# Performance work log

Hardware: AMD Instinct MI355X
Metric: run time of the kernel (lower is better)

## Reference

```python
import jax, jax.numpy as jnp
import numpy as np

B, S, H, F = 4, 2048, 1024, 4096
E, K = 8, 2


def setup_inputs() -> dict:
    key = jax.random.key(0)
    ks = jax.random.split(key, 8)
    s1 = 1.0 / np.sqrt(H)
    s2 = 1.0 / np.sqrt(F)
    return {
        "hidden_states": jax.random.normal(ks[0], (B, S, H), dtype=jnp.float32),
        "w1": jax.random.normal(ks[1], (E, H, F), dtype=jnp.float32) * s1,
        "b1": jnp.zeros((E, F), dtype=jnp.float32),
        "w2": jax.random.normal(ks[2], (E, F, H), dtype=jnp.float32) * s2,
        "b2": jnp.zeros((E, H), dtype=jnp.float32),
        "router_w": jax.random.normal(ks[3], (H, E), dtype=jnp.float32) * s1,
        "router_b": jnp.zeros((E,), dtype=jnp.float32),
    }


def reference(hidden_states, w1, b1, w2, b2, router_w, router_b):
    b, s, h = hidden_states.shape
    x = hidden_states.reshape(-1, h)              # [T, H]
    # --- router: softmax over expert logits, top-k, renormalize ---
    logits = x @ router_w + router_b              # [T, E]
    probs = jax.nn.softmax(logits, axis=-1)
    top_w, top_i = jax.lax.top_k(probs, K)        # [T, K]
    top_w = top_w / jnp.sum(top_w, axis=-1, keepdims=True)
    # --- dispatch/combine: per-expert FFN, weighted sum (same math as
    # gather/scatter loop in the torch module, expressed densely per expert) ---
    out = jnp.zeros_like(x)
    for e in range(E):
        we = jnp.sum(jnp.where(top_i == e, top_w, 0.0), axis=-1)   # [T]
        he = jax.nn.gelu(x @ w1[e] + b1[e]) @ w2[e] + b2[e]        # [T, H]
        out = out + we[:, None] * he
    return out.reshape(b, s, h)
```

## Files before the change

kernel.cpp:

```cpp
#include <hip/hip_runtime.h>
#include <cstdint>
#include <cstddef>

#define T_TOK 8192
#define HD 1024
#define FD 4096
#define NE 8
#define RCAP 17408

typedef __bf16 bf16_t;
typedef __bf16 bf16x8 __attribute__((ext_vector_type(8)));
typedef __bf16 bf16x4 __attribute__((ext_vector_type(4)));
typedef float floatx4 __attribute__((ext_vector_type(4)));

#define BM 128
#define BN 128
#define BK 64
#define LDS_STRIDE 72

__device__ __forceinline__ float gelu_tanh(float x) {
    float x3 = x * x * x;
    float t = tanhf(0.7978845608028654f * (x + 0.044715f * x3));
    return 0.5f * x * (1.0f + t);
}

__global__ __launch_bounds__(256) void transpose_conv_kernel(
    const float* __restrict__ in, bf16_t* __restrict__ out, int R, int C)
{
    __shared__ float tile[32][33];
    const int e = blockIdx.z;
    const int c0 = blockIdx.x * 32;
    const int r0 = blockIdx.y * 32;
    const float* src = in + (size_t)e * R * C;
    bf16_t* dst = out + (size_t)e * R * C;
    const int tx = threadIdx.x & 31;
    const int ty = threadIdx.x >> 5;
    #pragma unroll
    for (int i = ty; i < 32; i += 8)
        tile[i][tx] = src[(size_t)(r0 + i) * C + c0 + tx];
    __syncthreads();
    #pragma unroll
    for (int i = ty; i < 32; i += 8)
        dst[(size_t)(c0 + i) * R + r0 + tx] = (bf16_t)tile[tx][i];
}

__global__ __launch_bounds__(256) void router_kernel(
    const float* __restrict__ x, const float* __restrict__ rw,
    const float* __restrict__ rb,
    int* __restrict__ tok_e, float* __restrict__ tok_w, int* __restrict__ counts)
{
    const int t = blockIdx.x * 4 + (threadIdx.x >> 6);
    const int lane = threadIdx.x & 63;
    const float* xr = x + (size_t)t * HD;
    float acc[NE];
    #pragma unroll
    for (int e = 0; e < NE; ++e) acc[e] = 0.f;
    #pragma unroll 4
    for (int i = 0; i < HD / 64; ++i) {
        int h = lane + 64 * i;
        float xv = xr[h];
        const float4* w4 = (const float4*)(rw + (size_t)h * NE);
        float4 wa = w4[0], wb = w4[1];
        acc[0] += xv * wa.x; acc[1] += xv * wa.y;
        acc[2] += xv * wa.z; acc[3] += xv * wa.w;
        acc[4] += xv * wb.x; acc[5] += xv * wb.y;
        acc[6] += xv * wb.z; acc[7] += xv * wb.w;
    }
    #pragma unroll
    for (int s = 32; s > 0; s >>= 1)
        #pragma unroll
        for (int e = 0; e < NE; ++e)
            acc[e] += __shfl_xor(acc[e], s, 64);
    if (lane == 0) {
        float l[NE];
        #pragma unroll
        for (int e = 0; e < NE; ++e) l[e] = acc[e] + rb[e];
        int e1 = 0;
        #pragma unroll
        for (int e = 1; e < NE; ++e) if (l[e] > l[e1]) e1 = e;
        int e2 = (e1 == 0) ? 1 : 0;
        #pragma unroll
        for (int e = 0; e < NE; ++e) {
            if (e == e1 || e == e2) continue;
            if (l[e] > l[e2]) e2 = e;
        }
        float m = l[e1];
        float q1 = 1.0f;
        float q2 = expf(l[e2] - m);
        float inv = 1.0f / (q1 + q2);
        tok_e[t * 2]     = e1;
        tok_e[t * 2 + 1] = e2;
        tok_w[t * 2]     = q1 * inv;
        tok_w[t * 2 + 1] = q2 * inv;
        atomicAdd(&counts[e1], 1);
        atomicAdd(&counts[e2], 1);
    }
}

__global__ void offsets_kernel(const int* __restrict__ counts,
                               int* __restrict__ offsets, int* __restrict__ cursors)
{
    if (threadIdx.x == 0) {
        int cum = 0;
        for (int e = 0; e < NE; ++e) {
            offsets[e] = cum;
            cursors[e] = cum;
            cum += (counts[e] + BM - 1) & ~(BM - 1);
        }
    }
}

__global__ __launch_bounds__(256) void gather_kernel(
    const float* __restrict__ x, const int* __restrict__ tok_e,
    const float* __restrict__ tok_w, int* __restrict__ cursors,
    bf16_t* __restrict__ Xg, int* __restrict__ rows_token, float* __restrict__ rows_w)
{
    const int pair = blockIdx.x * 4 + (threadIdx.x >> 6);
    const int lane = threadIdx.x & 63;
    const int t = pair >> 1;
    int pos;
    if (lane == 0) {
        int e = tok_e[pair];
        pos = atomicAdd(&cursors[e], 1);
        rows_token[pos] = t;
        rows_w[pos] = tok_w[pair];
    }
    pos = __shfl(pos, 0, 64);
    const float4* src = (const float4*)(x + (size_t)t * HD);
    bf16_t* dst = Xg + (size_t)pos * HD;
    #pragma unroll
    for (int i = 0; i < HD / 256; ++i) {
        float4 v = src[lane + 64 * i];
        int base = (lane + 64 * i) * 4;
        bf16x4 o;
        o[0] = (bf16_t)v.x; o[1] = (bf16_t)v.y;
        o[2] = (bf16_t)v.z; o[3] = (bf16_t)v.w;
        *(bf16x4*)(dst + base) = o;
    }
}

template<int KDIM>
__device__ __forceinline__ void gemm_tile(
    const bf16_t* __restrict__ aG,
    const bf16_t* __restrict__ bG,
    bf16_t As[BM][LDS_STRIDE], bf16_t Bs[BN][LDS_STRIDE],
    floatx4 acc[4][4])
{
    const int tid = threadIdx.x;
    const int lane = tid & 63;
    const int wave = tid >> 6;
    const int quad = lane >> 4;
    const int l16 = lane & 15;
    const int wm = (wave & 1) * 64;
    const int wn = (wave >> 1) * 64;
    const int r0 = tid >> 3;
    const int c0 = (tid & 7) * 8;

    for (int k0 = 0; k0 < KDIM; k0 += BK) {
        #pragma unroll
        for (int p = 0; p < 4; ++p) {
            int r = p * 32 + r0;
            *(bf16x8*)(&As[r][c0]) = *(const bf16x8*)(aG + (size_t)r * KDIM + k0 + c0);
            *(bf16x8*)(&Bs[r][c0]) = *(const bf16x8*)(bG + (size_t)r * KDIM + k0 + c0);
        }
        __syncthreads();
        #pragma unroll
        for (int kk = 0; kk < BK; kk += 32) {
            bf16x8 af[4], bfr[4];
            #pragma unroll
            for (int i = 0; i < 4; ++i)
                af[i] = *(const bf16x8*)(&As[wm + i * 16 + l16][kk + quad * 8]);
            #pragma unroll
            for (int i = 0; i < 4; ++i)
                bfr[i] = *(const bf16x8*)(&Bs[wn + i * 16 + l16][kk + quad * 8]);
            #pragma unroll
            for (int i = 0; i < 4; ++i)
                #pragma unroll
                for (int j = 0; j < 4; ++j)
                    acc[i][j] = __builtin_amdgcn_mfma_f32_16x16x32_bf16(
                        af[i], bfr[j], acc[i][j], 0, 0, 0);
        }
        __syncthreads();
    }
}

__global__ __launch_bounds__(256) void ffn1_kernel(
    const bf16_t* __restrict__ Xg, const bf16_t* __restrict__ w1t,
    const float* __restrict__ b1, bf16_t* __restrict__ Hb,
    const int* __restrict__ counts, const int* __restrict__ offsets)
{
    const int e = blockIdx.z;
    const int cnt = counts[e];
    const int mtile = blockIdx.y;
    if (mtile * BM >= cnt) return;
    const int m_base = offsets[e] + mtile * BM;
    const int n_base = blockIdx.x * BN;

    __shared__ bf16_t As[BM][LDS_STRIDE];
    __shared__ bf16_t Bs[BN][LDS_STRIDE];
    floatx4 acc[4][4] = {};

    gemm_tile<HD>(Xg + (size_t)m_base * HD,
                  w1t + ((size_t)e * FD + n_base) * HD, As, Bs, acc);

    const int lane = threadIdx.x & 63;
    const int wave = threadIdx.x >> 6;
    const int quad = lane >> 4;
    const int l16 = lane & 15;
    const int wm = (wave & 1) * 64;
    const int wn = (wave >> 1) * 64;
    #pragma unroll
    for (int i = 0; i < 4; ++i) {
        int rl = wm + i * 16 + quad * 4;
        #pragma unroll
        for (int j = 0; j < 4; ++j) {
            int col = n_base + wn + j * 16 + l16;
            float bias = b1[e * FD + col];
            #pragma unroll
            for (int r = 0; r < 4; ++r) {
                float v = acc[i][j][r] + bias;
                Hb[(size_t)(m_base + rl + r) * FD + col] = (bf16_t)gelu_tanh(v);
            }
        }
    }
}

__global__ __launch_bounds__(256) void ffn2_kernel(
    const bf16_t* __restrict__ Hb, const bf16_t* __restrict__ w2t,
    const float* __restrict__ b2, float* __restrict__ out,
    const int* __restrict__ counts, const int* __restrict__ offsets,
    const int* __restrict__ rows_token, const float* __restrict__ rows_w)
{
    const int e = blockIdx.z;
    const int cnt = counts[e];
    const int mtile = blockIdx.y;
    if (mtile * BM >= cnt) return;
    const int m_base = offsets[e] + mtile * BM;
    const int n_base = blockIdx.x * BN;

    __shared__ bf16_t As[BM][LDS_STRIDE];
    __shared__ bf16_t Bs[BN][LDS_STRIDE];
    floatx4 acc[4][4] = {};

    gemm_tile<FD>(Hb + (size_t)m_base * FD,
                  w2t + ((size_t)e * HD + n_base) * FD, As, Bs, acc);

    const int lane = threadIdx.x & 63;
    const int wave = threadIdx.x >> 6;
    const int quad = lane >> 4;
    const int l16 = lane & 15;
    const int wm = (wave & 1) * 64;
    const int wn = (wave >> 1) * 64;
    const int loc_base = mtile * BM;
    #pragma unroll
    for (int i = 0; i < 4; ++i) {
        int rl = wm + i * 16 + quad * 4;
        #pragma unroll
        for (int j = 0; j < 4; ++j) {
            int col = n_base + wn + j * 16 + l16;
            float bias = b2[e * HD + col];
            #pragma unroll
            for (int r = 0; r < 4; ++r) {
                if (loc_base + rl + r < cnt) {
                    int gr = m_base + rl + r;
                    int token = rows_token[gr];
                    float wgt = rows_w[gr];
                    float v = acc[i][j][r] + bias;
                    atomicAdd(&out[(size_t)token * HD + col], wgt * v);
                }
            }
        }
    }
}

extern "C" void kernel_launch(void* const* d_in, const int* in_sizes, int n_in,
                              void* d_out, int out_size, void* d_ws, size_t ws_size,
                              hipStream_t stream)
{
    (void)in_sizes; (void)n_in; (void)ws_size;
    const float* x  = (const float*)d_in[0];
    const float* w1 = (const float*)d_in[1];
    const float* b1 = (const float*)d_in[2];
    const float* w2 = (const float*)d_in[3];
    const float* b2 = (const float*)d_in[4];
    const float* rw = (const float*)d_in[5];
    const float* rb = (const float*)d_in[6];
    float* out = (float*)d_out;

    char* ws = (char*)d_ws;
    size_t off = 0;
    auto alloc = [&](size_t bytes) -> void* {
        void* p = ws + off;
        off = (off + bytes + 255) & ~(size_t)255;
        return p;
    };
    int*    counts     = (int*)alloc(NE * sizeof(int));
    int*    cursors    = (int*)alloc(NE * sizeof(int));
    int*    offsets    = (int*)alloc(NE * sizeof(int));
    int*    tok_e      = (int*)alloc((size_t)T_TOK * 2 * sizeof(int));
    float*  tok_w      = (float*)alloc((size_t)T_TOK * 2 * sizeof(float));
    int*    rows_token = (int*)alloc((size_t)RCAP * sizeof(int));
    float*  rows_w     = (float*)alloc((size_t)RCAP * sizeof(float));
    bf16_t* Xg         = (bf16_t*)alloc((size_t)RCAP * HD * sizeof(bf16_t));
    bf16_t* Hb         = (bf16_t*)alloc((size_t)RCAP * FD * sizeof(bf16_t));
    bf16_t* w1t        = (bf16_t*)alloc((size_t)NE * FD * HD * sizeof(bf16_t));
    bf16_t* w2t        = (bf16_t*)alloc((size_t)NE * HD * FD * sizeof(bf16_t));

    hipMemsetAsync(counts, 0, NE * sizeof(int), stream);
    hipMemsetAsync(out, 0, (size_t)out_size * sizeof(float), stream);

    transpose_conv_kernel<<<dim3(FD / 32, HD / 32, NE), 256, 0, stream>>>(w1, w1t, HD, FD);
    transpose_conv_kernel<<<dim3(HD / 32, FD / 32, NE), 256, 0, stream>>>(w2, w2t, FD, HD);

    router_kernel<<<dim3(T_TOK / 4), 256, 0, stream>>>(x, rw, rb, tok_e, tok_w, counts);

    offsets_kernel<<<dim3(1), 64, 0, stream>>>(counts, offsets, cursors);

    gather_kernel<<<dim3(T_TOK * 2 / 4), 256, 0, stream>>>(
        x, tok_e, tok_w, cursors, Xg, rows_token, rows_w);

    ffn1_kernel<<<dim3(FD / BN, T_TOK / BM, NE), 256, 0, stream>>>(
        Xg, w1t, b1, Hb, counts, offsets);

    ffn2_kernel<<<dim3(HD / BN, T_TOK / BM, NE), 256, 0, stream>>>(
        Hb, w2t, b2, out, counts, offsets, rows_token, rows_w);
}
```

Measured before the change: 1.234 ms.

## Use async global-to-LDS loads, widen transpose tiles, swap grid axes

The GEMM tile loader now uses global_load_lds 16-byte async copies straight into unpadded LDS tiles, replacing the register-staged loads. The weight transpose/convert kernel moves to 64x64 tiles with float4 reads and 8-wide bf16 stores. The FFN grids swap the M and N axes so consecutive blocks walk token tiles, and the router drops a trivial multiply. Removing the LDS padding risks bank conflicts on the MFMA fragment reads, and per-lane 16-byte direct-to-LDS layout correctness depends on the intrinsic's addressing semantics.

```diff
diff --git a/kernel.cpp b/kernel.cpp
--- a/kernel.cpp
+++ b/kernel.cpp
@@ -16,7 +16,6 @@
 #define BM 128
 #define BN 128
 #define BK 64
-#define LDS_STRIDE 72
 
 __device__ __forceinline__ float gelu_tanh(float x) {
     float x3 = x * x * x;
@@ -24,24 +23,46 @@
     return 0.5f * x * (1.0f + t);
 }
 
+__device__ __forceinline__ void async_copy16(const void* g, void* l) {
+    __builtin_amdgcn_global_load_lds(
+        (const __attribute__((address_space(1))) void*)g,
+        (__attribute__((address_space(3))) void*)l,
+        16, 0, 0);
+}
+
 __global__ __launch_bounds__(256) void transpose_conv_kernel(
     const float* __restrict__ in, bf16_t* __restrict__ out, int R, int C)
 {
-    __shared__ float tile[32][33];
+    __shared__ float tile[64][65];
     const int e = blockIdx.z;
-    const int c0 = blockIdx.x * 32;
-    const int r0 = blockIdx.y * 32;
+    const int c0 = blockIdx.x * 64;
+    const int r0 = blockIdx.y * 64;
     const float* src = in + (size_t)e * R * C;
     bf16_t* dst = out + (size_t)e * R * C;
-    const int tx = threadIdx.x & 31;
-    const int ty = threadIdx.x >> 5;
-    #pragma unroll
-    for (int i = ty; i < 32; i += 8)
-        tile[i][tx] = src[(size_t)(r0 + i) * C + c0 + tx];
+
+    #pragma unroll
+    for (int it = 0; it < 4; ++it) {
+        int idx = threadIdx.x + it * 256;
+        int row = idx >> 4;
+        int c4  = (idx & 15) * 4;
+        float4 v = *(const float4*)(src + (size_t)(r0 + row) * C + c0 + c4);
+        tile[row][c4 + 0] = v.x;
+        tile[row][c4 + 1] = v.y;
+        tile[row][c4 + 2] = v.z;
+        tile[row][c4 + 3] = v.w;
+    }
     __syncthreads();
     #pragma unroll
-    for (int i = ty; i < 32; i += 8)
-        dst[(size_t)(c0 + i) * R + r0 + tx] = (bf16_t)tile[tx][i];
+    for (int it = 0; it < 2; ++it) {
+        int idx = threadIdx.x + it * 256;
+        int crow = idx >> 3;
+        int rch  = (idx & 7) * 8;
+        bf16x8 o;
+        #pragma unroll
+        for (int k = 0; k < 8; ++k)
+            o[k] = (bf16_t)tile[rch + k][crow];
+        *(bf16x8*)(dst + (size_t)(c0 + crow) * R + r0 + rch) = o;
+    }
 }
 
 __global__ __launch_bounds__(256) void router_kernel(
@@ -85,12 +106,11 @@
             if (l[e] > l[e2]) e2 = e;
         }
         float m = l[e1];
-        float q1 = 1.0f;
         float q2 = expf(l[e2] - m);
-        float inv = 1.0f / (q1 + q2);
+        float inv = 1.0f / (1.0f + q2);
         tok_e[t * 2]     = e1;
         tok_e[t * 2 + 1] = e2;
-        tok_w[t * 2]     = q1 * inv;
+        tok_w[t * 2]     = inv;
         tok_w[t * 2 + 1] = q2 * inv;
         atomicAdd(&counts[e1], 1);
         atomicAdd(&counts[e2], 1);
@@ -143,7 +163,7 @@
 __device__ __forceinline__ void gemm_tile(
     const bf16_t* __restrict__ aG,
     const bf16_t* __restrict__ bG,
-    bf16_t As[BM][LDS_STRIDE], bf16_t Bs[BN][LDS_STRIDE],
+    bf16_t (*As)[BK], bf16_t (*Bs)[BK],
     floatx4 acc[4][4])
 {
     const int tid = threadIdx.x;
@@ -153,15 +173,17 @@
     const int l16 = lane & 15;
     const int wm = (wave & 1) * 64;
     const int wn = (wave >> 1) * 64;
-    const int r0 = tid >> 3;
-    const int c0 = (tid & 7) * 8;
+    const int sr = lane >> 3;
+    const int sc = (lane & 7) * 8;
+
+    const bf16_t* aRow = aG + (size_t)(wave * 32 + sr) * KDIM + sc;
+    const bf16_t* bRow = bG + (size_t)(wave * 32 + sr) * KDIM + sc;
 
     for (int k0 = 0; k0 < KDIM; k0 += BK) {
         #pragma unroll
-        for (int p = 0; p < 4; ++p) {
-            int r = p * 32 + r0;
-            *(bf16x8*)(&As[r][c0]) = *(const bf16x8*)(aG + (size_t)r * KDIM + k0 + c0);
-            *(bf16x8*)(&Bs[r][c0]) = *(const bf16x8*)(bG + (size_t)r * KDIM + k0 + c0);
+        for (int i = 0; i < 4; ++i) {
+            async_copy16(aRow + (size_t)(i * 8) * KDIM + k0, &As[wave * 32 + i * 8][0]);
+            async_copy16(bRow + (size_t)(i * 8) * KDIM + k0, &Bs[wave * 32 + i * 8][0]);
         }
         __syncthreads();
         #pragma unroll
@@ -191,13 +213,13 @@
 {
     const int e = blockIdx.z;
     const int cnt = counts[e];
-    const int mtile = blockIdx.y;
+    const int mtile = blockIdx.x;
     if (mtile * BM >= cnt) return;
     const int m_base = offsets[e] + mtile * BM;
-    const int n_base = blockIdx.x * BN;
-
-    __shared__ bf16_t As[BM][LDS_STRIDE];
-    __shared__ bf16_t Bs[BN][LDS_STRIDE];
+    const int n_base = blockIdx.y * BN;
+
+    __shared__ bf16_t As[BM][BK];
+    __shared__ bf16_t Bs[BN][BK];
     floatx4 acc[4][4] = {};
 
     gemm_tile<HD>(Xg + (size_t)m_base * HD,
@@ -233,13 +255,13 @@
 {
     const int e = blockIdx.z;
     const int cnt = counts[e];
-    const int mtile = blockIdx.y;
+    const int mtile = blockIdx.x;
     if (mtile * BM >= cnt) return;
     const int m_base = offsets[e] + mtile * BM;
-    const int n_base = blockIdx.x * BN;
-
-    __shared__ bf16_t As[BM][LDS_STRIDE];
-    __shared__ bf16_t Bs[BN][LDS_STRIDE];
+    const int n_base = blockIdx.y * BN;
+
+    __shared__ bf16_t As[BM][BK];
+    __shared__ bf16_t Bs[BN][BK];
     floatx4 acc[4][4] = {};
 
     gemm_tile<FD>(Hb + (size_t)m_base * FD,
@@ -309,8 +331,8 @@
     hipMemsetAsync(counts, 0, NE * sizeof(int), stream);
     hipMemsetAsync(out, 0, (size_t)out_size * sizeof(float), stream);
 
-    transpose_conv_kernel<<<dim3(FD / 32, HD / 32, NE), 256, 0, stream>>>(w1, w1t, HD, FD);
-    transpose_conv_kernel<<<dim3(HD / 32, FD / 32, NE), 256, 0, stream>>>(w2, w2t, FD, HD);
+    transpose_conv_kernel<<<dim3(FD / 64, HD / 64, NE), 256, 0, stream>>>(w1, w1t, HD, FD);
+    transpose_conv_kernel<<<dim3(HD / 64, FD / 64, NE), 256, 0, stream>>>(w2, w2t, FD, HD);
 
     router_kernel<<<dim3(T_TOK / 4), 256, 0, stream>>>(x, rw, rb, tok_e, tok_w, counts);
 
@@ -319,9 +341,9 @@
     gather_kernel<<<dim3(T_TOK * 2 / 4), 256, 0, stream>>>(
         x, tok_e, tok_w, cursors, Xg, rows_token, rows_w);
 
-    ffn1_kernel<<<dim3(FD / BN, T_TOK / BM, NE), 256, 0, stream>>>(
+    ffn1_kernel<<<dim3(T_TOK / BM, FD / BN, NE), 256, 0, stream>>>(
         Xg, w1t, b1, Hb, counts, offsets);
 
-    ffn2_kernel<<<dim3(HD / BN, T_TOK / BM, NE), 256, 0, stream>>>(
+    ffn2_kernel<<<dim3(T_TOK / BM, HD / BN, NE), 256, 0, stream>>>(
         Hb, w2t, b2, out, counts, offsets, rows_token, rows_w);
 }
```

Measured after the change: 1.809 ms. 46.5% more time.
